# Performance work log

Hardware: AMD Instinct MI355X
Metric: run time of the kernel (lower is better)

The kernel has to match this reference:

```python
import jax, jax.numpy as jnp
import numpy as np

B, SQ, SKV = 4, 1024, 2048
DIM_Q, DIM_KV, NUM_HEADS, DIM_OUT = 512, 512, 8, 256
DIM_HEAD = DIM_Q // NUM_HEADS
NEG = -1e9


def setup_inputs() -> dict:
    key = jax.random.key(0)
    ks = jax.random.split(key, 14)
    s = 0.02
    return {
        "Q": jax.random.normal(ks[0], (B, SQ, DIM_Q), jnp.float32),
        "K": jax.random.normal(ks[1], (B, SKV, DIM_KV), jnp.float32),
        "V": jax.random.normal(ks[2], (B, SKV, DIM_KV), jnp.float32),
        "q_aff_mask": jax.random.uniform(ks[3], (B, SQ, SKV), jnp.float32),
        "q_binary_mask": jax.random.randint(ks[4], (B, SQ, SKV), 0, 2, jnp.int32),
        "kv_mask": jax.random.randint(ks[5], (B, SKV, 1), 0, 2, jnp.int32),
        "Wq": jax.random.normal(ks[6], (DIM_Q, DIM_Q), jnp.float32) * s,
        "bq": jnp.zeros((DIM_Q,), jnp.float32),
        "Wk": jax.random.normal(ks[7], (DIM_Q, DIM_KV), jnp.float32) * s,
        "bk": jnp.zeros((DIM_Q,), jnp.float32),
        "Wv": jax.random.normal(ks[8], (DIM_Q, DIM_KV), jnp.float32) * s,
        "bv": jnp.zeros((DIM_Q,), jnp.float32),
        "Wo": jax.random.normal(ks[9], (DIM_OUT, DIM_Q), jnp.float32) * s,
        "bo": jnp.zeros((DIM_OUT,), jnp.float32),
    }


def reference(Q, K, V, q_aff_mask, q_binary_mask, kv_mask,
              Wq, bq, Wk, bk, Wv, bv, Wo, bo):
    b, sq, _ = Q.shape
    skv = K.shape[1]
    # linear projections (torch Linear: x @ W.T + b)
    Qp = Q @ Wq.T + bq
    Kp = K @ Wk.T + bk
    Vp = V @ Wv.T + bv
    # split heads: [B, H, S, Dh]
    Qh = Qp.reshape(b, sq, NUM_HEADS, DIM_HEAD).transpose(0, 2, 1, 3)
    Kh = Kp.reshape(b, skv, NUM_HEADS, DIM_HEAD).transpose(0, 2, 1, 3)
    Vh = Vp.reshape(b, skv, NUM_HEADS, DIM_HEAD).transpose(0, 2, 1, 3)
    scale = 1.0 / jnp.sqrt(jnp.asarray(DIM_HEAD, Qh.dtype))
    scores = jnp.einsum("bhqd,bhkd->bhqk", Qh, Kh) * scale
    # kv_mask [B, Skv, 1]: True entries masked to -1e9, broadcast over heads/queries
    kv_bool = kv_mask[..., 0].astype(bool)[:, None, None, :]  # [B,1,1,Skv]
    scores = jnp.where(kv_bool, NEG, scores)
    # multiplicative affinity mask (applied AFTER kv masked_fill, as in source)
    scores = scores * q_aff_mask[:, None, :, :]
    # binary mask: True entries masked to -1e9
    qb_bool = q_binary_mask.astype(bool)[:, None, :, :]
    scores = jnp.where(qb_bool, NEG, scores)
    att_weights = jax.nn.softmax(scores, axis=-1)
    att_output = jnp.einsum("bhqk,bhkd->bhqd", att_weights, Vh)
    att_output = att_output.transpose(0, 2, 1, 3).reshape(b, sq, DIM_Q)
    att_output = att_output @ Wo.T + bo
    return att_output, att_weights
```

## Files before the change

### kernel.cpp

```cpp
#include <hip/hip_runtime.h>
#include <stdint.h>

typedef unsigned short u16;
typedef unsigned int   u32;
typedef __bf16 bf16x8 __attribute__((ext_vector_type(8)));
typedef float  f32x4  __attribute__((ext_vector_type(4)));
typedef u32    u32x4  __attribute__((ext_vector_type(4)));
typedef u16    u16x4  __attribute__((ext_vector_type(4)));

#define SQL  1024
#define SKV  2048
#define DQ   512
#define NH   8
#define DH   64
#define NEGC (-1e9f)
#define SCALEC 0.125f

#define OFF_QB  0ull
#define OFF_QP  2097152ull
#define OFF_KP  4194304ull
#define OFF_VPT 8388608ull
#define OFF_AP  12582912ull
#define OFF_BQ  14680064ull
#define OFF_BK  14942208ull
#define OFF_BV  15204352ull
#define OFF_BO  15466496ull
#define WS_NEED_BYTES (15597568ull * 2ull)

__device__ __forceinline__ u16 f2bf(float f) {
  u32 u = __float_as_uint(f);
  u32 r = u + 0x7fffu + ((u >> 16) & 1u);
  return (u16)(r >> 16);
}
__device__ __forceinline__ float bf2f(u16 h) {
  return __uint_as_float(((u32)h) << 16);
}
__device__ __forceinline__ bf16x8 ld16(const u16* p) {
  return __builtin_bit_cast(bf16x8, *(const u32x4*)p);
}
__device__ __forceinline__ f32x4 MFMA(bf16x8 a, bf16x8 b, f32x4 c) {
  return __builtin_amdgcn_mfma_f32_16x16x32_bf16(a, b, c, 0, 0, 0);
}
__device__ __forceinline__ void cvt8(const float* src, u16* dst, int t) {
  f32x4 a = ((const f32x4*)src)[2 * t], b = ((const f32x4*)src)[2 * t + 1];
  u32x4 o;
  o[0] = (u32)f2bf(a[0]) | ((u32)f2bf(a[1]) << 16);
  o[1] = (u32)f2bf(a[2]) | ((u32)f2bf(a[3]) << 16);
  o[2] = (u32)f2bf(b[0]) | ((u32)f2bf(b[1]) << 16);
  o[3] = (u32)f2bf(b[2]) | ((u32)f2bf(b[3]) << 16);
  *(u32x4*)(dst + 8 * t) = o;
}

__global__ void k_markf(float* outp, float val) {
  if (threadIdx.x == 0 && blockIdx.x == 0) outp[0] = val;
}

__global__ __launch_bounds__(256) void k_conv_x(
    const float* __restrict__ Q, const float* __restrict__ K, const float* __restrict__ V,
    u16* __restrict__ Qb, u16* __restrict__ Kb, u16* __restrict__ Vb)
{
  int t = blockIdx.x * 256 + threadIdx.x;
  if (t < 262144)       cvt8(Q, Qb, t);
  else if (t < 786432)  cvt8(K, Kb, t - 262144);
  else                  cvt8(V, Vb, t - 786432);
}

__global__ __launch_bounds__(256) void k_conv_w(
    const float* __restrict__ Wq, const float* __restrict__ Wk,
    const float* __restrict__ Wv, const float* __restrict__ Wo,
    u16* __restrict__ BQ, u16* __restrict__ BK, u16* __restrict__ BV, u16* __restrict__ BO)
{
  int t = blockIdx.x * 256 + threadIdx.x;
  if (t < 32768)        cvt8(Wq, BQ, t);
  else if (t < 65536)   cvt8(Wk, BK, t - 32768);
  else if (t < 98304)   cvt8(Wv, BV, t - 65536);
  else                  cvt8(Wo, BO, t - 98304);
}

template <typename OUT_T>
__global__ __launch_bounds__(256) void k_gemm(
    const u16* __restrict__ A, int lda,
    const u16* __restrict__ B2, int ldb,
    const float* __restrict__ bias,
    OUT_T* __restrict__ out, int ldo)
{
  __shared__ u16 As[128 * 72], Bs[128 * 72];
  const int tid = threadIdx.x;
  const int wid = tid >> 6, ln = tid & 63;
  const int l15 = ln & 15, lh = ln >> 4;
  const int m0 = blockIdx.x * 128, n0 = blockIdx.y * 128;
  const int wm = (wid & 1) * 64, wn = (wid >> 1) * 64;

  f32x4 acc[4][4];
#pragma unroll
  for (int mi = 0; mi < 4; ++mi)
#pragma unroll
    for (int ni = 0; ni < 4; ++ni) acc[mi][ni] = (f32x4){0.f, 0.f, 0.f, 0.f};

  for (int k0 = 0; k0 < 512; k0 += 64) {
#pragma unroll
    for (int s5 = 0; s5 < 4; ++s5) {
      int ci = s5 * 256 + tid;
      int row = ci >> 3, kc = ci & 7;
      *(u32x4*)(As + row * 72 + kc * 8) =
          *(const u32x4*)(A + (size_t)(m0 + row) * lda + k0 + kc * 8);
      *(u32x4*)(Bs + row * 72 + kc * 8) =
          *(const u32x4*)(B2 + (size_t)(n0 + row) * ldb + k0 + kc * 8);
    }
    __syncthreads();
    bf16x8 af[4][2], bfr[4][2];
#pragma unroll
    for (int mi = 0; mi < 4; ++mi) {
      int r = wm + mi * 16 + l15;
#pragma unroll
      for (int ks = 0; ks < 2; ++ks)
        af[mi][ks] = ld16(As + r * 72 + (ks * 4 + lh) * 8);
    }
#pragma unroll
    for (int ni = 0; ni < 4; ++ni) {
      int r = wn + ni * 16 + l15;
#pragma unroll
      for (int ks = 0; ks < 2; ++ks)
        bfr[ni][ks] = ld16(Bs + r * 72 + (ks * 4 + lh) * 8);
    }
#pragma unroll
    for (int mi = 0; mi < 4; ++mi)
#pragma unroll
      for (int ni = 0; ni < 4; ++ni) {
        acc[mi][ni] = MFMA(af[mi][0], bfr[ni][0], acc[mi][ni]);
        acc[mi][ni] = MFMA(af[mi][1], bfr[ni][1], acc[mi][ni]);
      }
    __syncthreads();
  }
  float bv[4];
#pragma unroll
  for (int ni = 0; ni < 4; ++ni) bv[ni] = bias[n0 + wn + ni * 16 + l15];
#pragma unroll
  for (int mi = 0; mi < 4; ++mi)
#pragma unroll
    for (int ni = 0; ni < 4; ++ni)
#pragma unroll
      for (int j = 0; j < 4; ++j) {
        float v = acc[mi][ni][j] + bv[ni];
        size_t idx = (size_t)(m0 + wm + mi * 16 + lh * 4 + j) * ldo + n0 + wn + ni * 16 + l15;
        if constexpr (sizeof(OUT_T) == 4) out[idx] = v;
        else                              out[idx] = f2bf(v);
      }
}

__global__ __launch_bounds__(256) void k_transpose(const u16* __restrict__ Vp, u16* __restrict__ VpT)
{
  __shared__ u16 T[64 * 72];
  const int bh = blockIdx.x, kt = blockIdx.y;
  const int b = bh >> 3, h = bh & 7;
  const int tid = threadIdx.x;
#pragma unroll
  for (int s = 0; s < 2; ++s) {
    int ci = s * 256 + tid;
    int row = ci >> 3, dc = ci & 7;
    *(u32x4*)(T + row * 72 + dc * 8) =
        *(const u32x4*)(Vp + (size_t)(b * 2048 + kt * 64 + row) * 512 + h * 64 + dc * 8);
  }
  __syncthreads();
#pragma unroll
  for (int s = 0; s < 2; ++s) {
    int ci = s * 256 + tid;
    int d = ci >> 3, kc = ci & 7;
    u32x4 v;
#pragma unroll
    for (int i = 0; i < 4; ++i) {
      u32 lo = T[(kc * 8 + 2 * i)     * 72 + d];
      u32 hi = T[(kc * 8 + 2 * i + 1) * 72 + d];
      v[i] = lo | (hi << 16);
    }
    *(u32x4*)(VpT + ((size_t)(b * 8 + h) * 64 + d) * 2048 + kt * 64 + kc * 8) = v;
  }
}

#define ASTR 68
#define PSTR 72
__global__ __launch_bounds__(512) void k_attn(
    const u16* __restrict__ Qp, const u16* __restrict__ Kp, const u16* __restrict__ VpT,
    const float* __restrict__ aff, const int* __restrict__ qbm, const int* __restrict__ kvm,
    float* __restrict__ wout, u16* __restrict__ AP)
{
  __shared__ float AffT[2][32][ASTR];
  __shared__ u16   Pf[8][32][PSTR];
  __shared__ float Ls[8][32];
  const int tid = threadIdx.x;
  const int w = tid >> 6, ln = tid & 63;
  const int l15 = ln & 15, lh = ln >> 4;
  const int combo = blockIdx.x & 7, rt = blockIdx.x >> 3;
  const int b = combo & 3, hg = combo >> 2;
  const int h = hg * 4 + (w & 3);
  const int kvhalf = w >> 2;
  const int kv0 = kvhalf * 1024;
  const int r0 = rt * 32;
  const int bh = b * NH + h;

  const int sHalf = tid >> 8;
  const int sRow  = (tid >> 3) & 31;
  const int sCol  = (tid & 7) * 8;
  const float* affS = aff + ((size_t)b * SQL + r0 + sRow) * SKV + sHalf * 1024 + sCol;
  const int*   qbS  = qbm + ((size_t)b * SQL + r0 + sRow) * SKV + sHalf * 1024 + sCol;

  bf16x8 qa[2][2];
#pragma unroll
  for (int qg = 0; qg < 2; ++qg) {
    const u16* qp = Qp + (size_t)(b * SQL + r0 + qg * 16 + l15) * DQ + h * DH + lh * 8;
    qa[qg][0] = ld16(qp); qa[qg][1] = ld16(qp + 32);
  }

  const int* kvb = kvm + (size_t)b * SKV;

  auto ldStage = [&](f32x4* st, int t) {
    f32x4 a0 = *(const f32x4*)(affS + t * 64);
    f32x4 a1 = *(const f32x4*)(affS + t * 64 + 4);
    u32x4 q0 = *(const u32x4*)(qbS + t * 64);
    u32x4 q1 = *(const u32x4*)(qbS + t * 64 + 4);
#pragma unroll
    for (int j = 0; j < 4; ++j) {
      st[0][j] = q0[j] ? -1.0f : a0[j];
      st[1][j] = q1[j] ? -1.0f : a1[j];
    }
  };
  auto wrStage = [&](const f32x4* st) {
    *(f32x4*)&AffT[sHalf][sRow][sCol]     = st[0];
    *(f32x4*)&AffT[sHalf][sRow][sCol + 4] = st[1];
  };

  auto compute_s = [&](int kb, f32x4 (*s)[4]) {
#pragma unroll
    for (int ni = 0; ni < 4; ++ni) {
      const u16* kp = Kp + (size_t)(b * SKV + kb + ni * 16 + l15) * DQ + h * DH + lh * 8;
      bf16x8 k0 = ld16(kp), k1 = ld16(kp + 32);
#pragma unroll
      for (int qg = 0; qg < 2; ++qg) {
        f32x4 z = (f32x4){0.f, 0.f, 0.f, 0.f};
        z = MFMA(k0, qa[qg][0], z);
        z = MFMA(k1, qa[qg][1], z);
        s[qg][ni] = z;
      }
      u32x4 km = *(const u32x4*)(kvb + kb + ni * 16 + lh * 4);
#pragma unroll
      for (int qg = 0; qg < 2; ++qg) {
        f32x4 f = *(const f32x4*)&AffT[kvhalf][qg * 16 + l15][ni * 16 + lh * 4];
#pragma unroll
        for (int j = 0; j < 4; ++j) {
          float v = s[qg][ni][j] * SCALEC;
          v = km[j] ? NEGC : v;
          v = (f[j] < 0.f) ? NEGC : v * f[j];
          s[qg][ni][j] = v;
        }
      }
    }
  };

  float sum[2] = {0.f, 0.f};
  auto stepA = [&](int t, f32x4* st, int tld) {
    wrStage(st);
    ldStage(st, tld);
    asm volatile("s_waitcnt lgkmcnt(0)" ::: "memory");
    __builtin_amdgcn_s_barrier();
    __builtin_amdgcn_sched_barrier(0);
    f32x4 s[2][4];
    compute_s(kv0 + t * 64, s);
#pragma unroll
    for (int qg = 0; qg < 2; ++qg)
#pragma unroll
      for (int ni = 0; ni < 4; ++ni)
#pragma unroll
        for (int j = 0; j < 4; ++j) sum[qg] += __expf(s[qg][ni][j]);
    __builtin_amdgcn_s_barrier();
  };

  f32x4 sA[2], sB[2];
  ldStage(sA, 0);
  ldStage(sB, 1);
  for (int tt = 0; tt < 8; ++tt) {
    stepA(2 * tt,     sA, (2 * tt + 2) & 15);
    stepA(2 * tt + 1, sB, (2 * tt + 3) & 15);
  }
#pragma unroll
  for (int qg = 0; qg < 2; ++qg) {
    sum[qg] += __shfl_xor(sum[qg], 16);
    sum[qg] += __shfl_xor(sum[qg], 32);
  }
  if (ln < 16) { Ls[w][ln] = sum[0]; Ls[w][16 + ln] = sum[1]; }
  __syncthreads();
  float rl[2];
  rl[0] = 1.0f / (sum[0] + Ls[w ^ 4][l15]);
  rl[1] = 1.0f / (sum[1] + Ls[w ^ 4][16 + l15]);

  f32x4 acc[2][4];
#pragma unroll
  for (int qg = 0; qg < 2; ++qg)
#pragma unroll
    for (int nd = 0; nd < 4; ++nd) acc[qg][nd] = (f32x4){0.f, 0.f, 0.f, 0.f};

  auto stepB = [&](int t, f32x4* st, int tld) {
    const int kb = kv0 + t * 64;
    wrStage(st);
    ldStage(st, tld);
    asm volatile("s_waitcnt lgkmcnt(0)" ::: "memory");
    __builtin_amdgcn_s_barrier();
    __builtin_amdgcn_sched_barrier(0);
    f32x4 s[2][4];
    compute_s(kb, s);
#pragma unroll
    for (int qg = 0; qg < 2; ++qg)
#pragma unroll
      for (int ni = 0; ni < 4; ++ni) {
        u16x4 pb;
#pragma unroll
        for (int j = 0; j < 4; ++j) pb[j] = f2bf(__expf(s[qg][ni][j]) * rl[qg]);
        *(u16x4*)&Pf[w][qg * 16 + l15][ni * 16 + lh * 4] = pb;
      }
    bf16x8 va[4], vb2[4];
#pragma unroll
    for (int nd = 0; nd < 4; ++nd) {
      const u16* vp = VpT + (size_t)(bh * DH + nd * 16 + l15) * SKV + kb + lh * 8;
      va[nd]  = ld16(vp);
      vb2[nd] = ld16(vp + 32);
    }
    asm volatile("s_waitcnt lgkmcnt(0)" ::: "memory");
    __builtin_amdgcn_sched_barrier(0);
    bf16x8 pa[2][2];
#pragma unroll
    for (int qg = 0; qg < 2; ++qg) {
      pa[qg][0] = ld16(&Pf[w][qg * 16 + l15][lh * 8]);
      pa[qg][1] = ld16(&Pf[w][qg * 16 + l15][32 + lh * 8]);
    }
#pragma unroll
    for (int qg = 0; qg < 2; ++qg)
#pragma unroll
      for (int nd = 0; nd < 4; ++nd) {
        acc[qg][nd] = MFMA(pa[qg][0], va[nd],  acc[qg][nd]);
        acc[qg][nd] = MFMA(pa[qg][1], vb2[nd], acc[qg][nd]);
      }
#pragma unroll
    for (int i = 0; i < 8; ++i) {
      const int row = (ln >> 4) + i * 4;
      const int col = (ln & 15) * 4;
      u16x4 pv = *(const u16x4*)&Pf[w][row][col];
      f32x4 wv;
#pragma unroll
      for (int j = 0; j < 4; ++j) wv[j] = bf2f(pv[j]);
      *(f32x4*)(wout + ((size_t)bh * SQL + r0 + row) * SKV + kb + col) = wv;
    }
    __builtin_amdgcn_s_barrier();
  };

  for (int tt = 0; tt < 8; ++tt) {
    stepB(2 * tt,     sA, (2 * tt + 2) & 15);
    stepB(2 * tt + 1, sB, (2 * tt + 3) & 15);
  }

  __syncthreads();
  float* AccXp = (float*)&Pf[0][0][0];
  if (w >= 4) {
#pragma unroll
    for (int qg = 0; qg < 2; ++qg)
#pragma unroll
      for (int nd = 0; nd < 4; ++nd)
        *(f32x4*)(AccXp + (size_t)((w - 4) * 64 + ln) * 32 + qg * 16 + nd * 4) = acc[qg][nd];
  }
  __syncthreads();
  if (w < 4) {
#pragma unroll
    for (int qg = 0; qg < 2; ++qg)
#pragma unroll
      for (int nd = 0; nd < 4; ++nd) {
        f32x4 o = *(const f32x4*)(AccXp + (size_t)(w * 64 + ln) * 32 + qg * 16 + nd * 4);
#pragma unroll
        for (int j = 0; j < 4; ++j)
          AP[(size_t)(b * SQL + r0 + qg * 16 + lh * 4 + j) * DQ + h * DH + nd * 16 + l15] =
              f2bf(acc[qg][nd][j] + o[j]);
      }
  }
}

extern "C" void kernel_launch(void* const* d_in, const int* in_sizes, int n_in,
                              void* d_out, int out_size, void* d_ws, size_t ws_size,
                              hipStream_t stream)
{
  const float* Q   = (const float*)d_in[0];
  const float* K   = (const float*)d_in[1];
  const float* V   = (const float*)d_in[2];
  const float* aff = (const float*)d_in[3];
  const int*   qb  = (const int*)d_in[4];
  const int*   kvm = (const int*)d_in[5];
  const float* Wq  = (const float*)d_in[6];
  const float* bq  = (const float*)d_in[7];
  const float* Wk  = (const float*)d_in[8];
  const float* bk  = (const float*)d_in[9];
  const float* Wv  = (const float*)d_in[10];
  const float* bv  = (const float*)d_in[11];
  const float* Wo  = (const float*)d_in[12];
  const float* bo  = (const float*)d_in[13];
  u16*   ws   = (u16*)d_ws;
  float* outF = (float*)d_out;
  float* wout = outF + 1048576;
  u16* Kb = (u16*)wout;
  u16* Vb = Kb + 4194304;
  u16* VP = Vb + 4194304;

  const int want[14] = {2097152, 4194304, 4194304, 8388608, 8388608, 8192,
                        262144, 512, 262144, 512, 262144, 512, 131072, 256};
  int bad = (n_in == 14) ? -1 : 14;
  if (bad < 0)
    for (int i = 0; i < 14; ++i)
      if (in_sizes[i] != want[i]) { bad = i; break; }
  if (bad >= 0) { k_markf<<<1, 64, 0, stream>>>(outF, 1024.0f * (160.0f + (float)bad)); return; }
  if (ws_size < WS_NEED_BYTES) { k_markf<<<1, 64, 0, stream>>>(outF, 180224.0f); return; }

  k_conv_x<<<5120, 256, 0, stream>>>(Q, K, V, ws + OFF_QB, Kb, Vb);
  k_conv_w<<<448, 256, 0, stream>>>(Wq, Wk, Wv, Wo, ws + OFF_BQ, ws + OFF_BK, ws + OFF_BV, ws + OFF_BO);
  k_gemm<u16><<<dim3(32, 4), 256, 0, stream>>>(ws + OFF_QB, 512, ws + OFF_BQ, 512, bq, ws + OFF_QP, 512);
  k_gemm<u16><<<dim3(64, 4), 256, 0, stream>>>(Kb, 512, ws + OFF_BK, 512, bk, ws + OFF_KP, 512);
  k_gemm<u16><<<dim3(64, 4), 256, 0, stream>>>(Vb, 512, ws + OFF_BV, 512, bv, VP, 512);
  k_transpose<<<dim3(32, 32), 256, 0, stream>>>(VP, ws + OFF_VPT);
  k_attn<<<dim3(256), 512, 0, stream>>>(ws + OFF_QP, ws + OFF_KP, ws + OFF_VPT,
                                        aff, qb, kvm, wout, ws + OFF_AP);
  k_gemm<float><<<dim3(32, 2), 256, 0, stream>>>(ws + OFF_AP, 512, ws + OFF_BO, 512, bo, outF, 256);
}
```

Baseline: 252.7 us.

## Prefetch K/V tiles into registers, precompute kv-mask bits, nontemporal weight stores

```diff
diff --git a/kernel.cpp b/kernel.cpp
--- a/kernel.cpp
+++ b/kernel.cpp
@@ -213,6 +213,24 @@
 
   const int* kvb = kvm + (size_t)b * SKV;
 
+  u32 kmBits[8];
+#pragma unroll
+  for (int t2 = 0; t2 < 8; ++t2) {
+    u32 bits = 0;
+#pragma unroll
+    for (int half = 0; half < 2; ++half) {
+      const int t = t2 * 2 + half;
+#pragma unroll
+      for (int ni = 0; ni < 4; ++ni) {
+        u32x4 km = *(const u32x4*)(kvb + kv0 + t * 64 + ni * 16 + lh * 4);
+#pragma unroll
+        for (int j = 0; j < 4; ++j)
+          bits |= (km[j] ? 1u : 0u) << (half * 16 + ni * 4 + j);
+      }
+    }
+    kmBits[t2] = bits;
+  }
+
   auto ldStage = [&](f32x4* st, int t) {
     f32x4 a0 = *(const f32x4*)(affS + t * 64);
     f32x4 a1 = *(const f32x4*)(affS + t * 64 + 4);
@@ -227,33 +245,6 @@
   auto wrStage = [&](const f32x4* st) {
     *(f32x4*)&AffT[sHalf][sRow][sCol]     = st[0];
     *(f32x4*)&AffT[sHalf][sRow][sCol + 4] = st[1];
-  };
-
-  auto compute_s = [&](int kb, f32x4 (*s)[4]) {
-#pragma unroll
-    for (int ni = 0; ni < 4; ++ni) {
-      const u16* kp = Kp + (size_t)(b * SKV + kb + ni * 16 + l15) * DQ + h * DH + lh * 8;
-      bf16x8 k0 = ld16(kp), k1 = ld16(kp + 32);
-#pragma unroll
-      for (int qg = 0; qg < 2; ++qg) {
-        f32x4 z = (f32x4){0.f, 0.f, 0.f, 0.f};
-        z = MFMA(k0, qa[qg][0], z);
-        z = MFMA(k1, qa[qg][1], z);
-        s[qg][ni] = z;
-      }
-      u32x4 km = *(const u32x4*)(kvb + kb + ni * 16 + lh * 4);
-#pragma unroll
-      for (int qg = 0; qg < 2; ++qg) {
-        f32x4 f = *(const f32x4*)&AffT[kvhalf][qg * 16 + l15][ni * 16 + lh * 4];
-#pragma unroll
-        for (int j = 0; j < 4; ++j) {
-          float v = s[qg][ni][j] * SCALEC;
-          v = km[j] ? NEGC : v;
-          v = (f[j] < 0.f) ? NEGC : v * f[j];
-          s[qg][ni][j] = v;
-        }
-      }
-    }
   };
 
   float sum[2] = {0.f, 0.f};
@@ -263,20 +254,34 @@
     asm volatile("s_waitcnt lgkmcnt(0)" ::: "memory");
     __builtin_amdgcn_s_barrier();
     __builtin_amdgcn_sched_barrier(0);
-    f32x4 s[2][4];
-    compute_s(kv0 + t * 64, s);
-#pragma unroll
-    for (int qg = 0; qg < 2; ++qg)
-#pragma unroll
-      for (int ni = 0; ni < 4; ++ni)
-#pragma unroll
-        for (int j = 0; j < 4; ++j) sum[qg] += __expf(s[qg][ni][j]);
+    const int kb = kv0 + t * 64;
+#pragma unroll
+    for (int ni = 0; ni < 4; ++ni) {
+      const u16* kp = Kp + (size_t)(b * SKV + kb + ni * 16 + l15) * DQ + h * DH + lh * 8;
+      bf16x8 k0 = ld16(kp), k1 = ld16(kp + 32);
+      const u32 bits = kmBits[t >> 1] >> (((t & 1) << 4) + ni * 4);
+#pragma unroll
+      for (int qg = 0; qg < 2; ++qg) {
+        f32x4 z = (f32x4){0.f, 0.f, 0.f, 0.f};
+        z = MFMA(k0, qa[qg][0], z);
+        z = MFMA(k1, qa[qg][1], z);
+        f32x4 f = *(const f32x4*)&AffT[kvhalf][qg * 16 + l15][ni * 16 + lh * 4];
+#pragma unroll
+        for (int j = 0; j < 4; ++j) {
+          float v = z[j] * SCALEC;
+          v = ((bits >> j) & 1) ? NEGC : v;
+          v = (f[j] < 0.f) ? NEGC : v * f[j];
+          sum[qg] += __expf(v);
+        }
+      }
+    }
     __builtin_amdgcn_s_barrier();
   };
 
   f32x4 sA[2], sB[2];
   ldStage(sA, 0);
   ldStage(sB, 1);
+#pragma unroll
   for (int tt = 0; tt < 8; ++tt) {
     stepA(2 * tt,     sA, (2 * tt + 2) & 15);
     stepA(2 * tt + 1, sB, (2 * tt + 3) & 15);
@@ -297,6 +302,15 @@
   for (int qg = 0; qg < 2; ++qg)
 #pragma unroll
     for (int nd = 0; nd < 4; ++nd) acc[qg][nd] = (f32x4){0.f, 0.f, 0.f, 0.f};
+
+  bf16x8 kC[4][2], vC[4][2];
+#pragma unroll
+  for (int ni = 0; ni < 4; ++ni) {
+    const u16* kp = Kp + (size_t)(b * SKV + kv0 + ni * 16 + l15) * DQ + h * DH + lh * 8;
+    kC[ni][0] = ld16(kp); kC[ni][1] = ld16(kp + 32);
+    const u16* vp = VpT + (size_t)(bh * DH + ni * 16 + l15) * SKV + kv0 + lh * 8;
+    vC[ni][0] = ld16(vp); vC[ni][1] = ld16(vp + 32);
+  }
 
   auto stepB = [&](int t, f32x4* st, int tld) {
     const int kb = kv0 + t * 64;
@@ -306,7 +320,24 @@
     __builtin_amdgcn_s_barrier();
     __builtin_amdgcn_sched_barrier(0);
     f32x4 s[2][4];
-    compute_s(kb, s);
+#pragma unroll
+    for (int ni = 0; ni < 4; ++ni) {
+      const u32 bits = kmBits[t >> 1] >> (((t & 1) << 4) + ni * 4);
+#pragma unroll
+      for (int qg = 0; qg < 2; ++qg) {
+        f32x4 z = (f32x4){0.f, 0.f, 0.f, 0.f};
+        z = MFMA(kC[ni][0], qa[qg][0], z);
+        z = MFMA(kC[ni][1], qa[qg][1], z);
+        f32x4 f = *(const f32x4*)&AffT[kvhalf][qg * 16 + l15][ni * 16 + lh * 4];
+#pragma unroll
+        for (int j = 0; j < 4; ++j) {
+          float v = z[j] * SCALEC;
+          v = ((bits >> j) & 1) ? NEGC : v;
+          v = (f[j] < 0.f) ? NEGC : v * f[j];
+          s[qg][ni][j] = v;
+        }
+      }
+    }
 #pragma unroll
     for (int qg = 0; qg < 2; ++qg)
 #pragma unroll
@@ -316,13 +347,6 @@
         for (int j = 0; j < 4; ++j) pb[j] = f2bf(__expf(s[qg][ni][j]) * rl[qg]);
         *(u16x4*)&Pf[w][qg * 16 + l15][ni * 16 + lh * 4] = pb;
       }
-    bf16x8 va[4], vb2[4];
-#pragma unroll
-    for (int nd = 0; nd < 4; ++nd) {
-      const u16* vp = VpT + (size_t)(bh * DH + nd * 16 + l15) * SKV + kb + lh * 8;
-      va[nd]  = ld16(vp);
-      vb2[nd] = ld16(vp + 32);
-    }
     asm volatile("s_waitcnt lgkmcnt(0)" ::: "memory");
     __builtin_amdgcn_sched_barrier(0);
     bf16x8 pa[2][2];
@@ -335,9 +359,18 @@
     for (int qg = 0; qg < 2; ++qg)
 #pragma unroll
       for (int nd = 0; nd < 4; ++nd) {
-        acc[qg][nd] = MFMA(pa[qg][0], va[nd],  acc[qg][nd]);
-        acc[qg][nd] = MFMA(pa[qg][1], vb2[nd], acc[qg][nd]);
-      }
+        acc[qg][nd] = MFMA(pa[qg][0], vC[nd][0], acc[qg][nd]);
+        acc[qg][nd] = MFMA(pa[qg][1], vC[nd][1], acc[qg][nd]);
+      }
+    const int kbN = kv0 + ((t + 1) & 15) * 64;
+#pragma unroll
+    for (int ni = 0; ni < 4; ++ni) {
+      const u16* kp = Kp + (size_t)(b * SKV + kbN + ni * 16 + l15) * DQ + h * DH + lh * 8;
+      kC[ni][0] = ld16(kp); kC[ni][1] = ld16(kp + 32);
+      const u16* vp = VpT + (size_t)(bh * DH + ni * 16 + l15) * SKV + kbN + lh * 8;
+      vC[ni][0] = ld16(vp); vC[ni][1] = ld16(vp + 32);
+    }
+    __builtin_amdgcn_sched_barrier(0);
 #pragma unroll
     for (int i = 0; i < 8; ++i) {
       const int row = (ln >> 4) + i * 4;
@@ -346,11 +379,12 @@
       f32x4 wv;
 #pragma unroll
       for (int j = 0; j < 4; ++j) wv[j] = bf2f(pv[j]);
-      *(f32x4*)(wout + ((size_t)bh * SQL + r0 + row) * SKV + kb + col) = wv;
+      __builtin_nontemporal_store(wv, (f32x4*)(wout + ((size_t)bh * SQL + r0 + row) * SKV + kb + col));
     }
     __builtin_amdgcn_s_barrier();
   };
 
+#pragma unroll
   for (int tt = 0; tt < 8; ++tt) {
     stepB(2 * tt,     sA, (2 * tt + 2) & 15);
     stepB(2 * tt + 1, sB, (2 * tt + 3) & 15);
```

Result: slower. 357.9 us (+41.6%).
